# Optimization experiments

Measured on AMD Instinct MI355X. Metric: run time of the kernel, lower is better.

Reference implementation:

```python
import jax, jax.numpy as jnp
import numpy as np

ROPE_BASE = 10000.0

def _rope_tables(seq_len, head_dim, dtype):
    inv_freq = 1.0 / (ROPE_BASE ** (jnp.arange(0, head_dim, 2, dtype=jnp.float32) / head_dim))
    t = jnp.arange(seq_len, dtype=jnp.float32)
    freqs = jnp.einsum('s,d->sd', t, inv_freq)  # [S, D/2]
    return jnp.cos(freqs).astype(dtype), jnp.sin(freqs).astype(dtype)

def _apply_rope(x, cos, sin):
    # x: [B, H, S, D]; cos/sin: [S, D/2]
    half = x.shape[-1] // 2
    x1, x2 = x[..., :half], x[..., half:]
    c = cos[None, None, :, :]
    s = sin[None, None, :, :]
    return jnp.concatenate([x1 * c - x2 * s, x1 * s + x2 * c], axis=-1)

def setup_inputs() -> dict:
    key = jax.random.key(0)
    k1, k2, k3 = jax.random.split(key, 3)
    B, S, dim = 4, 2048, 1024
    x = jax.random.normal(k1, (B, S, dim), dtype=jnp.float32)
    Wqkv = jax.random.normal(k2, (3 * dim, dim), dtype=jnp.float32) * (1.0 / np.sqrt(dim))
    Wout = jax.random.normal(k3, (dim, dim), dtype=jnp.float32) * (1.0 / np.sqrt(dim))
    mask = jnp.tril(jnp.ones((S, S), dtype=bool))[None, None, :, :]  # causal [1,1,S,S]
    return {"x": x, "mask": mask, "Wqkv": Wqkv, "Wout": Wout, "n_heads": 16}

def reference(x, mask, Wqkv, Wout, n_heads):
    B, S, dim = x.shape
    H = n_heads
    D = dim // H
    qkv = jnp.einsum('bsd,ed->bse', x, Wqkv)             # [B,S,3*dim]
    qkv = qkv.reshape(B, S, 3, H, D)
    q = jnp.transpose(qkv[:, :, 0], (0, 2, 1, 3))        # [B,H,S,D]
    k = jnp.transpose(qkv[:, :, 1], (0, 2, 1, 3))
    v = jnp.transpose(qkv[:, :, 2], (0, 2, 1, 3))
    cos, sin = _rope_tables(S, D, x.dtype)
    q = _apply_rope(q, cos, sin)
    k = _apply_rope(k, cos, sin)
    scale = 1.0 / np.sqrt(D).astype(np.float32)
    scores = jnp.einsum('bhsd,bhtd->bhst', q, k) * scale  # [B,H,S,S]
    scores = jnp.where(mask, scores, -jnp.inf)
    attn = jax.nn.softmax(scores, axis=-1)
    out = jnp.einsum('bhst,bhtd->bhsd', attn, v)          # [B,H,S,D]
    out = jnp.transpose(out, (0, 2, 1, 3)).reshape(B, S, dim)
    return jnp.einsum('bsd,ed->bse', out, Wout)
```

## Files before the change

kernel.cpp:

```cpp
#include <hip/hip_runtime.h>
#include <math.h>


typedef __attribute__((ext_vector_type(8))) __bf16 bf16x8;
typedef __attribute__((ext_vector_type(8))) short  short8;
typedef __attribute__((ext_vector_type(4))) short  s16x4;
typedef __attribute__((ext_vector_type(4))) float  f32x4;

#define MFMA16(a, b, c) __builtin_amdgcn_mfma_f32_16x16x32_bf16((a), (b), (c), 0, 0, 0)

static constexpr int    BATCH = 4;
static constexpr int    SEQ   = 2048;
static constexpr int    DIM   = 1024;
static constexpr int    NH    = 16;
static constexpr int    HD    = 64;
static constexpr size_t BHSD  = (size_t)BATCH * NH * SEQ * HD;
static constexpr float  NEGINF = -1e9f;
static constexpr int    PS_LD  = 72;

__device__ __forceinline__ short f2bf(float f) {
    union { float f; unsigned u; } v; v.f = f;
    unsigned r = v.u + 0x7fffu + ((v.u >> 16) & 1u);
    return (short)(r >> 16);
}

__device__ __forceinline__ short8 cvt8(const f32x4 lo, const f32x4 hi) {
    short8 r;
    r[0] = f2bf(lo[0]); r[1] = f2bf(lo[1]); r[2] = f2bf(lo[2]); r[3] = f2bf(lo[3]);
    r[4] = f2bf(hi[0]); r[5] = f2bf(hi[1]); r[6] = f2bf(hi[2]); r[7] = f2bf(hi[3]);
    return r;
}

template <bool F32>
__device__ __forceinline__ short8 ld8(const void* p, size_t row, int K, int k) {
    if constexpr (F32) {
        const float* f = (const float*)p;
        f32x4 lo = *(const f32x4*)&f[row * (size_t)K + k];
        f32x4 hi = *(const f32x4*)&f[row * (size_t)K + k + 4];
        return cvt8(lo, hi);
    } else {
        const short* s = (const short*)p;
        return *(const short8*)&s[row * (size_t)K + k];
    }
}

__device__ __forceinline__ void gload16(const void* g, void* lds) {
    __builtin_amdgcn_global_load_lds(
        (const __attribute__((address_space(1))) void*)g,
        (__attribute__((address_space(3))) void*)lds, 16, 0, 0);
}

__global__ __launch_bounds__(256) void prep_kernel(
    const float* __restrict__ X, const float* __restrict__ Wq,
    const float* __restrict__ Wo, short* __restrict__ Xb,
    short* __restrict__ Wqb, short* __restrict__ Wob,
    float* __restrict__ cosT, float* __restrict__ sinT) {
    const int stride = gridDim.x * blockDim.x;
    for (int idx = blockIdx.x * blockDim.x + threadIdx.x; idx < 3211264; idx += stride) {
        if (idx < 3145728) {
            const float* src; short* dst; int off;
            if (idx < 2097152)      { src = X;  dst = Xb;  off = idx; }
            else if (idx < 2883584) { src = Wq; dst = Wqb; off = idx - 2097152; }
            else                    { src = Wo; dst = Wob; off = idx - 2883584; }
            f32x4 v = *(const f32x4*)&src[(size_t)off * 4];
            s16x4 r;
            r[0] = f2bf(v[0]); r[1] = f2bf(v[1]); r[2] = f2bf(v[2]); r[3] = f2bf(v[3]);
            *(s16x4*)&dst[(size_t)off * 4] = r;
        } else {
            int r = idx - 3145728;
            int s = r >> 5, d = r & 31;
            float ang = (float)s * __expf(-0.28782313662425574f * (float)d);
            float sn, cs;
            sincosf(ang, &sn, &cs);
            cosT[r] = cs; sinT[r] = sn;
        }
    }
}

template <bool AF32, bool BF32>
__device__ __forceinline__ void gemm128_core(
    const void* __restrict__ A, const void* __restrict__ B, int K,
    short* As, short* Bs, int bm, int bn, f32x4 acc[4][4]) {
    const int tid  = threadIdx.x;
    const int lane = tid & 63;
    const int wave = tid >> 6;
    const int quad = lane >> 4;
    const int col  = lane & 15;
    const int wm   = (wave & 1) * 64;
    const int wn   = (wave >> 1) * 64;

    const int r0 = tid >> 2;
    const int r1 = (tid + 256) >> 2;
    const int ko = (tid & 3) * 8;

#pragma unroll
    for (int i = 0; i < 4; ++i)
#pragma unroll
        for (int j = 0; j < 4; ++j) acc[i][j] = f32x4{0.f, 0.f, 0.f, 0.f};

#pragma unroll 1
    for (int k0 = 0; k0 < K; k0 += 32) {
        short8 a0 = ld8<AF32>(A, (size_t)(bm + r0), K, k0 + ko);
        short8 a1 = ld8<AF32>(A, (size_t)(bm + r1), K, k0 + ko);
        short8 b0 = ld8<BF32>(B, (size_t)(bn + r0), K, k0 + ko);
        short8 b1 = ld8<BF32>(B, (size_t)(bn + r1), K, k0 + ko);
        __syncthreads();
        *(short8*)&As[tid * 8]         = a0;
        *(short8*)&As[(tid + 256) * 8] = a1;
        *(short8*)&Bs[tid * 8]         = b0;
        *(short8*)&Bs[(tid + 256) * 8] = b1;
        __syncthreads();

        bf16x8 af[4], bfr[4];
#pragma unroll
        for (int i = 0; i < 4; ++i)
            af[i] = *(const bf16x8*)&As[(wm + i * 16 + col) * 32 + quad * 8];
#pragma unroll
        for (int j = 0; j < 4; ++j)
            bfr[j] = *(const bf16x8*)&Bs[(wn + j * 16 + col) * 32 + quad * 8];
#pragma unroll
        for (int i = 0; i < 4; ++i)
#pragma unroll
            for (int j = 0; j < 4; ++j)
                acc[i][j] = MFMA16(af[i], bfr[j], acc[i][j]);
    }
}

__device__ __forceinline__ void gemm128_lds(
    const short* __restrict__ A, const short* __restrict__ B, int K,
    short* As, short* Bs, int bm, int bn, f32x4 acc[4][4]) {
    const int tid  = threadIdx.x;
    const int lane = tid & 63;
    const int wave = tid >> 6;
    const int quad = lane >> 4;
    const int col  = lane & 15;
    const int wm   = (wave & 1) * 64;
    const int wn   = (wave >> 1) * 64;

    const int r0 = tid >> 2;
    const int r1 = r0 + 64;
    const int ko = (tid & 3) * 8;

    const short* A0 = &A[(size_t)(bm + r0) * K + ko];
    const short* A1 = &A[(size_t)(bm + r1) * K + ko];
    const short* B0 = &B[(size_t)(bn + r0) * K + ko];
    const short* B1 = &B[(size_t)(bn + r1) * K + ko];

    short* As0 = &As[wave * 512];
    short* As1 = &As[2048 + wave * 512];
    short* Bs0 = &Bs[wave * 512];
    short* Bs1 = &Bs[2048 + wave * 512];

#pragma unroll
    for (int i = 0; i < 4; ++i)
#pragma unroll
        for (int j = 0; j < 4; ++j) acc[i][j] = f32x4{0.f, 0.f, 0.f, 0.f};

#pragma unroll 1
    for (int k0 = 0; k0 < K; k0 += 32) {
        __syncthreads();
        gload16(A0 + k0, As0);
        gload16(A1 + k0, As1);
        gload16(B0 + k0, Bs0);
        gload16(B1 + k0, Bs1);
        __syncthreads();

        bf16x8 af[4], bfr[4];
#pragma unroll
        for (int i = 0; i < 4; ++i)
            af[i] = *(const bf16x8*)&As[(wm + i * 16 + col) * 32 + quad * 8];
#pragma unroll
        for (int j = 0; j < 4; ++j)
            bfr[j] = *(const bf16x8*)&Bs[(wn + j * 16 + col) * 32 + quad * 8];
#pragma unroll
        for (int i = 0; i < 4; ++i)
#pragma unroll
            for (int j = 0; j < 4; ++j)
                acc[i][j] = MFMA16(af[i], bfr[j], acc[i][j]);
    }
}

template <bool PRE>
__global__ __launch_bounds__(256, 2) void qkv_rope_kernel(
    const void* __restrict__ X, const void* __restrict__ W,
    const float* __restrict__ cosT, const float* __restrict__ sinT,
    short* __restrict__ Qo, short* __restrict__ Ko, short* __restrict__ VT) {
    __shared__ __align__(16) short As[128 * 32];
    __shared__ __align__(16) short Bs[128 * 32];
    const int bm = blockIdx.y * 128, bn = blockIdx.x * 128;
    const int lane = threadIdx.x & 63, wave = threadIdx.x >> 6;
    const int quad = lane >> 4, col = lane & 15;
    const int wm = (wave & 1) * 64, wn = (wave >> 1) * 64;

    f32x4 acc[4][4];
    if constexpr (PRE)
        gemm128_lds((const short*)X, (const short*)W, 1024, As, Bs, bm, bn, acc);
    else
        gemm128_core<true, true>(X, W, 1024, As, Bs, bm, bn, acc);

    const int n0    = bn + wn;
    const int which = n0 >> 10;
    const int h     = (n0 >> 6) & 15;

    if (which == 2) {
#pragma unroll
        for (int i = 0; i < 4; ++i) {
            int    m = bm + wm + i * 16 + quad * 4;
            int    b = m >> 11, s = m & 2047;
            size_t rowb = (size_t)(b * NH + h) * HD;
#pragma unroll
            for (int j = 0; j < 4; ++j) {
                int   d = j * 16 + col;
                s16x4 pk;
                pk[0] = f2bf(acc[i][j][0]); pk[1] = f2bf(acc[i][j][1]);
                pk[2] = f2bf(acc[i][j][2]); pk[3] = f2bf(acc[i][j][3]);
                *(s16x4*)&VT[(rowb + d) * SEQ + s] = pk;
            }
        }
    } else {
        short* dst = which ? Ko : Qo;
#pragma unroll
        for (int i = 0; i < 4; ++i)
#pragma unroll
            for (int reg = 0; reg < 4; ++reg) {
                int    m = bm + wm + i * 16 + quad * 4 + reg;
                int    b = m >> 11, s = m & 2047;
                size_t base = ((size_t)(b * NH + h) * SEQ + s) * HD;
#pragma unroll
                for (int j = 0; j < 2; ++j) {
                    int   d1 = j * 16 + col;
                    float sn, cs;
                    if constexpr (PRE) {
                        cs = cosT[(s << 5) + d1];
                        sn = sinT[(s << 5) + d1];
                    } else {
                        float inv = __expf(-0.28782313662425574f * (float)d1);
                        sincosf((float)s * inv, &sn, &cs);
                    }
                    float x1 = acc[i][j][reg];
                    float x2 = acc[i][j + 2][reg];
                    dst[base + d1]      = f2bf(x1 * cs - x2 * sn);
                    dst[base + d1 + 32] = f2bf(x1 * sn + x2 * cs);
                }
            }
    }
}

__global__ __launch_bounds__(256, 2) void attn_kernel(
    const short* __restrict__ Q, const short* __restrict__ K,
    const short* __restrict__ VT, short* __restrict__ att) {
    const int b = blockIdx.z, h = blockIdx.y;
    const int tid = threadIdx.x, wave = tid >> 6, lane = tid & 63;
    const int quad = lane >> 4, col = lane & 15;
    const size_t hoff = (size_t)(b * NH + h) * SEQ * HD;
    const short* Qp  = Q + hoff;
    const short* Kp  = K + hoff;
    const short* VTp = VT + hoff;

    __shared__ __align__(16) short Kt[64 * 64];
    __shared__ __align__(16) short Vt[64 * 64];
    __shared__ __align__(16) short Ps[4 * 16 * PS_LD];

    const int r0 = tid >> 3;
    const int r1 = r0 + 32;
    const int c8 = (tid & 7) * 8;
    const int cs = c8 ^ ((r0 & 7) << 3);
    const int swc = (col & 7) << 3;
    const int cA  = (quad * 8) ^ swc;
    const int cB  = (32 + quad * 8) ^ swc;
    short* Pw = &Ps[wave * 16 * PS_LD];

#pragma unroll 1
    for (int pass = 0; pass < 2; ++pass) {
        const int qt = pass ? 31 - (int)blockIdx.x : (int)blockIdx.x;
        const int q0 = qt * 64 + wave * 16;

        bf16x8 aq0 = *(const bf16x8*)&Qp[(q0 + col) * HD + quad * 8];
        bf16x8 aq1 = *(const bf16x8*)&Qp[(q0 + col) * HD + 32 + quad * 8];

        float m_i[4], l_i[4];
        f32x4 o[4];
#pragma unroll
        for (int r = 0; r < 4; ++r) { m_i[r] = NEGINF; l_i[r] = 0.f; o[r] = f32x4{0.f, 0.f, 0.f, 0.f}; }

        short8 ka = *(const short8*)&Kp[r0 * HD + c8];
        short8 kb = *(const short8*)&Kp[r1 * HD + c8];
        short8 va = *(const short8*)&VTp[(size_t)r0 * SEQ + c8];
        short8 vb = *(const short8*)&VTp[(size_t)r1 * SEQ + c8];

#pragma unroll 1
        for (int t = 0; t <= qt; ++t) {
            const int kt = t * 64;
            __syncthreads();
            *(short8*)&Kt[r0 * 64 + cs] = ka;
            *(short8*)&Kt[r1 * 64 + cs] = kb;
            *(short8*)&Vt[r0 * 64 + cs] = va;
            *(short8*)&Vt[r1 * 64 + cs] = vb;
            __syncthreads();

            if (t < qt) {
                const int kn = kt + 64;
                ka = *(const short8*)&Kp[(kn + r0) * HD + c8];
                kb = *(const short8*)&Kp[(kn + r1) * HD + c8];
                va = *(const short8*)&VTp[(size_t)r0 * SEQ + kn + c8];
                vb = *(const short8*)&VTp[(size_t)r1 * SEQ + kn + c8];
            }

            float p[4][4];
#pragma unroll
            for (int jn = 0; jn < 4; ++jn) {
                f32x4  s  = f32x4{0.f, 0.f, 0.f, 0.f};
                bf16x8 b0 = *(const bf16x8*)&Kt[(jn * 16 + col) * 64 + cA];
                bf16x8 b1 = *(const bf16x8*)&Kt[(jn * 16 + col) * 64 + cB];
                s = MFMA16(aq0, b0, s);
                s = MFMA16(aq1, b1, s);
                if (t == qt) {
#pragma unroll
                    for (int reg = 0; reg < 4; ++reg) {
                        int qr = wave * 16 + quad * 4 + reg;
                        int kc = jn * 16 + col;
                        p[jn][reg] = (kc <= qr) ? s[reg] * 0.125f : NEGINF;
                    }
                } else {
#pragma unroll
                    for (int reg = 0; reg < 4; ++reg) p[jn][reg] = s[reg] * 0.125f;
                }
            }

            float lm[4];
#pragma unroll
            for (int reg = 0; reg < 4; ++reg)
                lm[reg] = fmaxf(fmaxf(p[0][reg], p[1][reg]), fmaxf(p[2][reg], p[3][reg]));
            int ok = (lm[0] <= m_i[0] + 8.f) & (lm[1] <= m_i[1] + 8.f) &
                     (lm[2] <= m_i[2] + 8.f) & (lm[3] <= m_i[3] + 8.f);
            if (__all(ok)) {
#pragma unroll
                for (int reg = 0; reg < 4; ++reg) {
                    float rs = 0.f;
#pragma unroll
                    for (int jn = 0; jn < 4; ++jn) {
                        p[jn][reg] = __expf(p[jn][reg] - m_i[reg]);
                        rs += p[jn][reg];
                    }
                    l_i[reg] += rs;
                }
            } else {
                float alpha[4];
#pragma unroll
                for (int reg = 0; reg < 4; ++reg) {
                    float mx = lm[reg];
#pragma unroll
                    for (int off = 8; off >= 1; off >>= 1) mx = fmaxf(mx, __shfl_xor(mx, off, 64));
                    float mn   = fmaxf(m_i[reg], mx);
                    alpha[reg] = __expf(m_i[reg] - mn);
                    float rs = 0.f;
#pragma unroll
                    for (int jn = 0; jn < 4; ++jn) {
                        p[jn][reg] = __expf(p[jn][reg] - mn);
                        rs += p[jn][reg];
                    }
                    l_i[reg] = l_i[reg] * alpha[reg] + rs;
                    m_i[reg] = mn;
                }
#pragma unroll
                for (int jd = 0; jd < 4; ++jd)
#pragma unroll
                    for (int reg = 0; reg < 4; ++reg) o[jd][reg] *= alpha[reg];
            }

#pragma unroll
            for (int jn = 0; jn < 4; ++jn)
#pragma unroll
                for (int reg = 0; reg < 4; ++reg)
                    Pw[(quad * 4 + reg) * PS_LD + jn * 16 + col] = f2bf(p[jn][reg]);

            bf16x8 ap0 = *(const bf16x8*)&Pw[col * PS_LD + quad * 8];
            bf16x8 ap1 = *(const bf16x8*)&Pw[col * PS_LD + 32 + quad * 8];
#pragma unroll
            for (int jd = 0; jd < 4; ++jd) {
                bf16x8 bv0 = *(const bf16x8*)&Vt[(jd * 16 + col) * 64 + cA];
                bf16x8 bv1 = *(const bf16x8*)&Vt[(jd * 16 + col) * 64 + cB];
                o[jd] = MFMA16(ap0, bv0, o[jd]);
                o[jd] = MFMA16(ap1, bv1, o[jd]);
            }
        }

#pragma unroll
        for (int off = 8; off >= 1; off >>= 1)
#pragma unroll
            for (int reg = 0; reg < 4; ++reg)
                l_i[reg] += __shfl_xor(l_i[reg], off, 64);
        float inv_l[4];
#pragma unroll
        for (int reg = 0; reg < 4; ++reg) inv_l[reg] = 1.f / l_i[reg];
#pragma unroll
        for (int jd = 0; jd < 4; ++jd)
#pragma unroll
            for (int reg = 0; reg < 4; ++reg) {
                int s = q0 + quad * 4 + reg;
                att[((size_t)(b * SEQ + s)) * DIM + h * HD + jd * 16 + col] =
                    f2bf(o[jd][reg] * inv_l[reg]);
            }
    }
}

template <bool PRE>
__global__ __launch_bounds__(256, 2) void out_gemm_kernel(
    const short* __restrict__ A, const void* __restrict__ W,
    float* __restrict__ out) {
    __shared__ __align__(16) short As[128 * 32];
    __shared__ __align__(16) short Bs[128 * 32];
    const int bm = blockIdx.y * 128, bn = blockIdx.x * 128;
    const int lane = threadIdx.x & 63, wave = threadIdx.x >> 6;
    const int quad = lane >> 4, col = lane & 15;
    const int wm = (wave & 1) * 64, wn = (wave >> 1) * 64;

    f32x4 acc[4][4];
    if constexpr (PRE)
        gemm128_lds(A, (const short*)W, 1024, As, Bs, bm, bn, acc);
    else
        gemm128_core<false, true>(A, W, 1024, As, Bs, bm, bn, acc);

#pragma unroll
    for (int i = 0; i < 4; ++i)
#pragma unroll
        for (int reg = 0; reg < 4; ++reg) {
            int    m    = bm + wm + i * 16 + quad * 4 + reg;
            size_t base = (size_t)m * DIM + bn + wn;
#pragma unroll
            for (int j = 0; j < 4; ++j)
                out[base + j * 16 + col] = acc[i][j][reg];
        }
}

extern "C" void kernel_launch(void* const* d_in, const int* in_sizes, int n_in,
                              void* d_out, int out_size, void* d_ws, size_t ws_size,
                              hipStream_t stream) {
    const float* x    = nullptr;
    const float* Wqkv = nullptr;
    const float* Wout = nullptr;
    for (int i = 0; i < n_in; ++i) {
        switch (in_sizes[i]) {
            case 8388608: x    = (const float*)d_in[i]; break;
            case 3145728: Wqkv = (const float*)d_in[i]; break;
            case 1048576: Wout = (const float*)d_in[i]; break;
            default: break;
        }
    }
    if (!x || !Wqkv || !Wout) return;

    short* Q  = (short*)d_ws;
    short* K  = Q + BHSD;
    short* VT = K + BHSD;
    float* out = (float*)d_out;

    const size_t need_pre = (size_t)4 * BHSD * sizeof(short)
                          + BHSD * sizeof(short)
                          + (size_t)3145728 * sizeof(short)
                          + (size_t)1048576 * sizeof(short)
                          + (size_t)2 * 65536 * sizeof(float);

    if (ws_size >= need_pre) {
        short* att  = VT + BHSD;
        short* Xb   = att + BHSD;
        short* Wqb  = Xb + BHSD;
        short* Wob  = Wqb + 3145728;
        float* cosT = (float*)(Wob + 1048576);
        float* sinT = cosT + 65536;

        prep_kernel<<<dim3(2048), 256, 0, stream>>>(x, Wqkv, Wout, Xb, Wqb, Wob, cosT, sinT);
        qkv_rope_kernel<true><<<dim3(24, 64), 256, 0, stream>>>(Xb, Wqb, cosT, sinT, Q, K, VT);
        attn_kernel<<<dim3(16, NH, BATCH), 256, 0, stream>>>(Q, K, VT, att);
        out_gemm_kernel<true><<<dim3(8, 64), 256, 0, stream>>>(att, Wob, out);
    } else {
        qkv_rope_kernel<false><<<dim3(24, 64), 256, 0, stream>>>(
            x, Wqkv, nullptr, nullptr, Q, K, VT);

        const bool direct = ws_size >= (size_t)4 * BHSD * sizeof(short);
        short* att_dst = direct ? (VT + BHSD) : (short*)d_out;
        attn_kernel<<<dim3(16, NH, BATCH), 256, 0, stream>>>(Q, K, VT, att_dst);

        short* att = att_dst;
        if (!direct) {
            att = (short*)d_ws;
            hipMemcpyAsync(att, att_dst, BHSD * sizeof(short), hipMemcpyDeviceToDevice, stream);
        }
        out_gemm_kernel<false><<<dim3(8, 64), 256, 0, stream>>>(att, Wout, out);
    }
}
```

Before: 297.2 us.

## Widen attention blocks to 128 query rows with 8 waves sharing K/V tiles

The attention kernel now runs 512 threads (8 waves) per block, covering 128 query rows, so each K/V tile staged in shared memory is reused by twice as many waves and each thread loads one row instead of two. The grid halves to 8 blocks per head, with paired early/late tiles still balancing causal work. Waves whose queries sit entirely before a key tile skip its compute but still join the barriers. s_setprio is raised around the MFMA sections to favour matrix issue. In exchange, diagonal tiles leave some waves idle, there are fewer blocks overall, and the larger block may raise register pressure.

```diff
diff --git a/kernel.cpp b/kernel.cpp
--- a/kernel.cpp
+++ b/kernel.cpp
@@ -246,7 +246,7 @@
     }
 }
 
-__global__ __launch_bounds__(256, 2) void attn_kernel(
+__global__ __launch_bounds__(512, 2) void attn_kernel(
     const short* __restrict__ Q, const short* __restrict__ K,
     const short* __restrict__ VT, short* __restrict__ att) {
     const int b = blockIdx.z, h = blockIdx.y;
@@ -259,12 +259,11 @@
 
     __shared__ __align__(16) short Kt[64 * 64];
     __shared__ __align__(16) short Vt[64 * 64];
-    __shared__ __align__(16) short Ps[4 * 16 * PS_LD];
-
-    const int r0 = tid >> 3;
-    const int r1 = r0 + 32;
+    __shared__ __align__(16) short Ps[8 * 16 * PS_LD];
+
+    const int r  = tid >> 3;
     const int c8 = (tid & 7) * 8;
-    const int cs = c8 ^ ((r0 & 7) << 3);
+    const int cs = c8 ^ ((r & 7) << 3);
     const int swc = (col & 7) << 3;
     const int cA  = (quad * 8) ^ swc;
     const int cB  = (32 + quad * 8) ^ swc;
@@ -272,8 +271,9 @@
 
 #pragma unroll 1
     for (int pass = 0; pass < 2; ++pass) {
-        const int qt = pass ? 31 - (int)blockIdx.x : (int)blockIdx.x;
-        const int q0 = qt * 64 + wave * 16;
+        const int qt   = pass ? 15 - (int)blockIdx.x : (int)blockIdx.x;
+        const int q0   = qt * 128 + wave * 16;
+        const int tmax = 2 * qt + 1;
 
         bf16x8 aq0 = *(const bf16x8*)&Qp[(q0 + col) * HD + quad * 8];
         bf16x8 aq1 = *(const bf16x8*)&Qp[(q0 + col) * HD + 32 + quad * 8];
@@ -281,32 +281,29 @@
         float m_i[4], l_i[4];
         f32x4 o[4];
 #pragma unroll
-        for (int r = 0; r < 4; ++r) { m_i[r] = NEGINF; l_i[r] = 0.f; o[r] = f32x4{0.f, 0.f, 0.f, 0.f}; }
-
-        short8 ka = *(const short8*)&Kp[r0 * HD + c8];
-        short8 kb = *(const short8*)&Kp[r1 * HD + c8];
-        short8 va = *(const short8*)&VTp[(size_t)r0 * SEQ + c8];
-        short8 vb = *(const short8*)&VTp[(size_t)r1 * SEQ + c8];
+        for (int rr = 0; rr < 4; ++rr) { m_i[rr] = NEGINF; l_i[rr] = 0.f; o[rr] = f32x4{0.f, 0.f, 0.f, 0.f}; }
+
+        short8 ka = *(const short8*)&Kp[r * HD + c8];
+        short8 va = *(const short8*)&VTp[(size_t)r * SEQ + c8];
 
 #pragma unroll 1
-        for (int t = 0; t <= qt; ++t) {
+        for (int t = 0; t <= tmax; ++t) {
             const int kt = t * 64;
             __syncthreads();
-            *(short8*)&Kt[r0 * 64 + cs] = ka;
-            *(short8*)&Kt[r1 * 64 + cs] = kb;
-            *(short8*)&Vt[r0 * 64 + cs] = va;
-            *(short8*)&Vt[r1 * 64 + cs] = vb;
+            *(short8*)&Kt[r * 64 + cs] = ka;
+            *(short8*)&Vt[r * 64 + cs] = va;
             __syncthreads();
 
-            if (t < qt) {
+            if (t < tmax) {
                 const int kn = kt + 64;
-                ka = *(const short8*)&Kp[(kn + r0) * HD + c8];
-                kb = *(const short8*)&Kp[(kn + r1) * HD + c8];
-                va = *(const short8*)&VTp[(size_t)r0 * SEQ + kn + c8];
-                vb = *(const short8*)&VTp[(size_t)r1 * SEQ + kn + c8];
-            }
+                ka = *(const short8*)&Kp[(kn + r) * HD + c8];
+                va = *(const short8*)&VTp[(size_t)r * SEQ + kn + c8];
+            }
+
+            if (kt > q0 + 15) continue;
 
             float p[4][4];
+            __builtin_amdgcn_s_setprio(1);
 #pragma unroll
             for (int jn = 0; jn < 4; ++jn) {
                 f32x4  s  = f32x4{0.f, 0.f, 0.f, 0.f};
@@ -314,11 +311,11 @@
                 bf16x8 b1 = *(const bf16x8*)&Kt[(jn * 16 + col) * 64 + cB];
                 s = MFMA16(aq0, b0, s);
                 s = MFMA16(aq1, b1, s);
-                if (t == qt) {
+                if (t >= 2 * qt) {
 #pragma unroll
                     for (int reg = 0; reg < 4; ++reg) {
-                        int qr = wave * 16 + quad * 4 + reg;
-                        int kc = jn * 16 + col;
+                        int qr = q0 + quad * 4 + reg;
+                        int kc = kt + jn * 16 + col;
                         p[jn][reg] = (kc <= qr) ? s[reg] * 0.125f : NEGINF;
                     }
                 } else {
@@ -326,6 +323,7 @@
                     for (int reg = 0; reg < 4; ++reg) p[jn][reg] = s[reg] * 0.125f;
                 }
             }
+            __builtin_amdgcn_s_setprio(0);
 
             float lm[4];
 #pragma unroll
@@ -376,6 +374,7 @@
 
             bf16x8 ap0 = *(const bf16x8*)&Pw[col * PS_LD + quad * 8];
             bf16x8 ap1 = *(const bf16x8*)&Pw[col * PS_LD + 32 + quad * 8];
+            __builtin_amdgcn_s_setprio(1);
 #pragma unroll
             for (int jd = 0; jd < 4; ++jd) {
                 bf16x8 bv0 = *(const bf16x8*)&Vt[(jd * 16 + col) * 64 + cA];
@@ -383,6 +382,7 @@
                 o[jd] = MFMA16(ap0, bv0, o[jd]);
                 o[jd] = MFMA16(ap1, bv1, o[jd]);
             }
+            __builtin_amdgcn_s_setprio(0);
         }
 
 #pragma unroll
@@ -470,7 +470,7 @@
 
         prep_kernel<<<dim3(2048), 256, 0, stream>>>(x, Wqkv, Wout, Xb, Wqb, Wob, cosT, sinT);
         qkv_rope_kernel<true><<<dim3(24, 64), 256, 0, stream>>>(Xb, Wqb, cosT, sinT, Q, K, VT);
-        attn_kernel<<<dim3(16, NH, BATCH), 256, 0, stream>>>(Q, K, VT, att);
+        attn_kernel<<<dim3(8, NH, BATCH), 512, 0, stream>>>(Q, K, VT, att);
         out_gemm_kernel<true><<<dim3(8, 64), 256, 0, stream>>>(att, Wob, out);
     } else {
         qkv_rope_kernel<false><<<dim3(24, 64), 256, 0, stream>>>(
@@ -478,7 +478,7 @@
 
         const bool direct = ws_size >= (size_t)4 * BHSD * sizeof(short);
         short* att_dst = direct ? (VT + BHSD) : (short*)d_out;
-        attn_kernel<<<dim3(16, NH, BATCH), 256, 0, stream>>>(Q, K, VT, att_dst);
+        attn_kernel<<<dim3(8, NH, BATCH), 512, 0, stream>>>(Q, K, VT, att_dst);
 
         short* att = att_dst;
         if (!direct) {
```

Measured after the change: 299.3 us. No clear change (+0.7%).

## Enlarge attention query tile to 128 rows, two 16-row subtiles per wave

Applied to the files above, without the earlier changes.

Each wave now processes 32 query rows (two MFMA subtiles) against each staged K/V tile, so a block covers 128 queries and the grid halves to 8 blocks per head. Each K/V LDS tile is reused twice as much, and tiles fully above the diagonal for a wave are skipped. It also raises wave priority around the MFMA sections with s_setprio. In exchange it uses more registers and LDS per block and launches fewer blocks, which may reduce occupancy and make the causal load balance coarser.

```diff
diff --git a/kernel.cpp b/kernel.cpp
--- a/kernel.cpp
+++ b/kernel.cpp
@@ -259,7 +259,7 @@
 
     __shared__ __align__(16) short Kt[64 * 64];
     __shared__ __align__(16) short Vt[64 * 64];
-    __shared__ __align__(16) short Ps[4 * 16 * PS_LD];
+    __shared__ __align__(16) short Ps[4 * 32 * PS_LD];
 
     const int r0 = tid >> 3;
     const int r1 = r0 + 32;
@@ -268,20 +268,30 @@
     const int swc = (col & 7) << 3;
     const int cA  = (quad * 8) ^ swc;
     const int cB  = (32 + quad * 8) ^ swc;
-    short* Pw = &Ps[wave * 16 * PS_LD];
+    short* Pw = &Ps[wave * 32 * PS_LD];
 
 #pragma unroll 1
     for (int pass = 0; pass < 2; ++pass) {
-        const int qt = pass ? 31 - (int)blockIdx.x : (int)blockIdx.x;
-        const int q0 = qt * 64 + wave * 16;
-
-        bf16x8 aq0 = *(const bf16x8*)&Qp[(q0 + col) * HD + quad * 8];
-        bf16x8 aq1 = *(const bf16x8*)&Qp[(q0 + col) * HD + 32 + quad * 8];
-
-        float m_i[4], l_i[4];
-        f32x4 o[4];
-#pragma unroll
-        for (int r = 0; r < 4; ++r) { m_i[r] = NEGINF; l_i[r] = 0.f; o[r] = f32x4{0.f, 0.f, 0.f, 0.f}; }
+        const int qt   = pass ? 15 - (int)blockIdx.x : (int)blockIdx.x;
+        const int q0   = qt * 128 + wave * 32;
+        const int tmax = 2 * qt + 1;
+
+        bf16x8 aq[2][2];
+#pragma unroll
+        for (int s2 = 0; s2 < 2; ++s2) {
+            aq[s2][0] = *(const bf16x8*)&Qp[(q0 + s2 * 16 + col) * HD + quad * 8];
+            aq[s2][1] = *(const bf16x8*)&Qp[(q0 + s2 * 16 + col) * HD + 32 + quad * 8];
+        }
+
+        float m_i[2][4], l_i[2][4];
+        f32x4 o[2][4];
+#pragma unroll
+        for (int s2 = 0; s2 < 2; ++s2)
+#pragma unroll
+            for (int rr = 0; rr < 4; ++rr) {
+                m_i[s2][rr] = NEGINF; l_i[s2][rr] = 0.f;
+                o[s2][rr] = f32x4{0.f, 0.f, 0.f, 0.f};
+            }
 
         short8 ka = *(const short8*)&Kp[r0 * HD + c8];
         short8 kb = *(const short8*)&Kp[r1 * HD + c8];
@@ -289,7 +299,7 @@
         short8 vb = *(const short8*)&VTp[(size_t)r1 * SEQ + c8];
 
 #pragma unroll 1
-        for (int t = 0; t <= qt; ++t) {
+        for (int t = 0; t <= tmax; ++t) {
             const int kt = t * 64;
             __syncthreads();
             *(short8*)&Kt[r0 * 64 + cs] = ka;
@@ -298,7 +308,7 @@
             *(short8*)&Vt[r1 * 64 + cs] = vb;
             __syncthreads();
 
-            if (t < qt) {
+            if (t < tmax) {
                 const int kn = kt + 64;
                 ka = *(const short8*)&Kp[(kn + r0) * HD + c8];
                 kb = *(const short8*)&Kp[(kn + r1) * HD + c8];
@@ -306,101 +316,128 @@
                 vb = *(const short8*)&VTp[(size_t)r1 * SEQ + kn + c8];
             }
 
-            float p[4][4];
+            if (kt > q0 + 31) continue;
+
+            float p[2][4][4];
+            __builtin_amdgcn_s_setprio(1);
 #pragma unroll
             for (int jn = 0; jn < 4; ++jn) {
-                f32x4  s  = f32x4{0.f, 0.f, 0.f, 0.f};
                 bf16x8 b0 = *(const bf16x8*)&Kt[(jn * 16 + col) * 64 + cA];
                 bf16x8 b1 = *(const bf16x8*)&Kt[(jn * 16 + col) * 64 + cB];
-                s = MFMA16(aq0, b0, s);
-                s = MFMA16(aq1, b1, s);
-                if (t == qt) {
+#pragma unroll
+                for (int s2 = 0; s2 < 2; ++s2) {
+                    f32x4 s = f32x4{0.f, 0.f, 0.f, 0.f};
+                    s = MFMA16(aq[s2][0], b0, s);
+                    s = MFMA16(aq[s2][1], b1, s);
+                    if (t >= 2 * qt) {
+#pragma unroll
+                        for (int reg = 0; reg < 4; ++reg) {
+                            int qr = q0 + s2 * 16 + quad * 4 + reg;
+                            int kc = kt + jn * 16 + col;
+                            p[s2][jn][reg] = (kc <= qr) ? s[reg] * 0.125f : NEGINF;
+                        }
+                    } else {
+#pragma unroll
+                        for (int reg = 0; reg < 4; ++reg)
+                            p[s2][jn][reg] = s[reg] * 0.125f;
+                    }
+                }
+            }
+            __builtin_amdgcn_s_setprio(0);
+
+#pragma unroll
+            for (int s2 = 0; s2 < 2; ++s2) {
+                float lm[4];
+#pragma unroll
+                for (int reg = 0; reg < 4; ++reg)
+                    lm[reg] = fmaxf(fmaxf(p[s2][0][reg], p[s2][1][reg]),
+                                    fmaxf(p[s2][2][reg], p[s2][3][reg]));
+                int ok = (lm[0] <= m_i[s2][0] + 8.f) & (lm[1] <= m_i[s2][1] + 8.f) &
+                         (lm[2] <= m_i[s2][2] + 8.f) & (lm[3] <= m_i[s2][3] + 8.f);
+                if (__all(ok)) {
 #pragma unroll
                     for (int reg = 0; reg < 4; ++reg) {
-                        int qr = wave * 16 + quad * 4 + reg;
-                        int kc = jn * 16 + col;
-                        p[jn][reg] = (kc <= qr) ? s[reg] * 0.125f : NEGINF;
+                        float rs = 0.f;
+#pragma unroll
+                        for (int jn = 0; jn < 4; ++jn) {
+                            p[s2][jn][reg] = __expf(p[s2][jn][reg] - m_i[s2][reg]);
+                            rs += p[s2][jn][reg];
+                        }
+                        l_i[s2][reg] += rs;
                     }
                 } else {
-#pragma unroll
-                    for (int reg = 0; reg < 4; ++reg) p[jn][reg] = s[reg] * 0.125f;
+                    float alpha[4];
+#pragma unroll
+                    for (int reg = 0; reg < 4; ++reg) {
+                        float mx = lm[reg];
+#pragma unroll
+                        for (int off = 8; off >= 1; off >>= 1)
+                            mx = fmaxf(mx, __shfl_xor(mx, off, 64));
+                        float mn   = fmaxf(m_i[s2][reg], mx);
+                        alpha[reg] = __expf(m_i[s2][reg] - mn);
+                        float rs = 0.f;
+#pragma unroll
+                        for (int jn = 0; jn < 4; ++jn) {
+                            p[s2][jn][reg] = __expf(p[s2][jn][reg] - mn);
+                            rs += p[s2][jn][reg];
+                        }
+                        l_i[s2][reg] = l_i[s2][reg] * alpha[reg] + rs;
+                        m_i[s2][reg] = mn;
+                    }
+#pragma unroll
+                    for (int jd = 0; jd < 4; ++jd)
+#pragma unroll
+                        for (int reg = 0; reg < 4; ++reg)
+                            o[s2][jd][reg] *= alpha[reg];
                 }
-            }
-
-            float lm[4];
-#pragma unroll
-            for (int reg = 0; reg < 4; ++reg)
-                lm[reg] = fmaxf(fmaxf(p[0][reg], p[1][reg]), fmaxf(p[2][reg], p[3][reg]));
-            int ok = (lm[0] <= m_i[0] + 8.f) & (lm[1] <= m_i[1] + 8.f) &
-                     (lm[2] <= m_i[2] + 8.f) & (lm[3] <= m_i[3] + 8.f);
-            if (__all(ok)) {
-#pragma unroll
-                for (int reg = 0; reg < 4; ++reg) {
-                    float rs = 0.f;
-#pragma unroll
-                    for (int jn = 0; jn < 4; ++jn) {
-                        p[jn][reg] = __expf(p[jn][reg] - m_i[reg]);
-                        rs += p[jn][reg];
-                    }
-                    l_i[reg] += rs;
-                }
-            } else {
-                float alpha[4];
-#pragma unroll
-                for (int reg = 0; reg < 4; ++reg) {
-                    float mx = lm[reg];
-#pragma unroll
-                    for (int off = 8; off >= 1; off >>= 1) mx = fmaxf(mx, __shfl_xor(mx, off, 64));
-                    float mn   = fmaxf(m_i[reg], mx);
-                    alpha[reg] = __expf(m_i[reg] - mn);
-                    float rs = 0.f;
-#pragma unroll
-                    for (int jn = 0; jn < 4; ++jn) {
-                        p[jn][reg] = __expf(p[jn][reg] - mn);
-                        rs += p[jn][reg];
-                    }
-                    l_i[reg] = l_i[reg] * alpha[reg] + rs;
-                    m_i[reg] = mn;
-                }
-#pragma unroll
-                for (int jd = 0; jd < 4; ++jd)
-#pragma unroll
-                    for (int reg = 0; reg < 4; ++reg) o[jd][reg] *= alpha[reg];
-            }
-
-#pragma unroll
-            for (int jn = 0; jn < 4; ++jn)
-#pragma unroll
-                for (int reg = 0; reg < 4; ++reg)
-                    Pw[(quad * 4 + reg) * PS_LD + jn * 16 + col] = f2bf(p[jn][reg]);
-
-            bf16x8 ap0 = *(const bf16x8*)&Pw[col * PS_LD + quad * 8];
-            bf16x8 ap1 = *(const bf16x8*)&Pw[col * PS_LD + 32 + quad * 8];
+
+#pragma unroll
+                for (int jn = 0; jn < 4; ++jn)
+#pragma unroll
+                    for (int reg = 0; reg < 4; ++reg)
+                        Pw[(s2 * 16 + quad * 4 + reg) * PS_LD + jn * 16 + col] =
+                            f2bf(p[s2][jn][reg]);
+            }
+
+            bf16x8 ap[2][2];
+#pragma unroll
+            for (int s2 = 0; s2 < 2; ++s2) {
+                ap[s2][0] = *(const bf16x8*)&Pw[(s2 * 16 + col) * PS_LD + quad * 8];
+                ap[s2][1] = *(const bf16x8*)&Pw[(s2 * 16 + col) * PS_LD + 32 + quad * 8];
+            }
+            __builtin_amdgcn_s_setprio(1);
 #pragma unroll
             for (int jd = 0; jd < 4; ++jd) {
                 bf16x8 bv0 = *(const bf16x8*)&Vt[(jd * 16 + col) * 64 + cA];
                 bf16x8 bv1 = *(const bf16x8*)&Vt[(jd * 16 + col) * 64 + cB];
-                o[jd] = MFMA16(ap0, bv0, o[jd]);
-                o[jd] = MFMA16(ap1, bv1, o[jd]);
-            }
-        }
-
-#pragma unroll
-        for (int off = 8; off >= 1; off >>= 1)
-#pragma unroll
-            for (int reg = 0; reg < 4; ++reg)
-                l_i[reg] += __shfl_xor(l_i[reg], off, 64);
-        float inv_l[4];
-#pragma unroll
-        for (int reg = 0; reg < 4; ++reg) inv_l[reg] = 1.f / l_i[reg];
-#pragma unroll
-        for (int jd = 0; jd < 4; ++jd)
-#pragma unroll
-            for (int reg = 0; reg < 4; ++reg) {
-                int s = q0 + quad * 4 + reg;
-                att[((size_t)(b * SEQ + s)) * DIM + h * HD + jd * 16 + col] =
-                    f2bf(o[jd][reg] * inv_l[reg]);
-            }
+#pragma unroll
+                for (int s2 = 0; s2 < 2; ++s2) {
+                    o[s2][jd] = MFMA16(ap[s2][0], bv0, o[s2][jd]);
+                    o[s2][jd] = MFMA16(ap[s2][1], bv1, o[s2][jd]);
+                }
+            }
+            __builtin_amdgcn_s_setprio(0);
+        }
+
+#pragma unroll
+        for (int s2 = 0; s2 < 2; ++s2) {
+#pragma unroll
+            for (int off = 8; off >= 1; off >>= 1)
+#pragma unroll
+                for (int reg = 0; reg < 4; ++reg)
+                    l_i[s2][reg] += __shfl_xor(l_i[s2][reg], off, 64);
+            float inv_l[4];
+#pragma unroll
+            for (int reg = 0; reg < 4; ++reg) inv_l[reg] = 1.f / l_i[s2][reg];
+#pragma unroll
+            for (int jd = 0; jd < 4; ++jd)
+#pragma unroll
+                for (int reg = 0; reg < 4; ++reg) {
+                    int s = q0 + s2 * 16 + quad * 4 + reg;
+                    att[((size_t)(b * SEQ + s)) * DIM + h * HD + jd * 16 + col] =
+                        f2bf(o[s2][jd][reg] * inv_l[reg]);
+                }
+        }
     }
 }
 
@@ -470,7 +507,7 @@
 
         prep_kernel<<<dim3(2048), 256, 0, stream>>>(x, Wqkv, Wout, Xb, Wqb, Wob, cosT, sinT);
         qkv_rope_kernel<true><<<dim3(24, 64), 256, 0, stream>>>(Xb, Wqb, cosT, sinT, Q, K, VT);
-        attn_kernel<<<dim3(16, NH, BATCH), 256, 0, stream>>>(Q, K, VT, att);
+        attn_kernel<<<dim3(8, NH, BATCH), 256, 0, stream>>>(Q, K, VT, att);
         out_gemm_kernel<true><<<dim3(8, 64), 256, 0, stream>>>(att, Wob, out);
     } else {
         qkv_rope_kernel<false><<<dim3(24, 64), 256, 0, stream>>>(
@@ -478,7 +515,7 @@
 
         const bool direct = ws_size >= (size_t)4 * BHSD * sizeof(short);
         short* att_dst = direct ? (VT + BHSD) : (short*)d_out;
-        attn_kernel<<<dim3(16, NH, BATCH), 256, 0, stream>>>(Q, K, VT, att_dst);
+        attn_kernel<<<dim3(8, NH, BATCH), 256, 0, stream>>>(Q, K, VT, att_dst);
 
         short* att = att_dst;
         if (!direct) {
```

New measurement: 287.5 us. 3.3% less time.
